# Kernel tuning notes

Hardware: AMD Instinct MI355X
Metric: run time of the kernel (lower is better)

## Reference

```python
import jax, jax.numpy as jnp
import numpy as np
from jax import lax

V, E, H, S = 50000, 512, 512, 16384


def setup_inputs() -> dict:
    key = jax.random.key(0)
    ks = jax.random.split(key, 10)
    sc_e = 1.0 / np.sqrt(E)
    sc_h = 1.0 / np.sqrt(H)
    return {
        "x": jax.random.randint(ks[0], (S,), 0, V, dtype=jnp.int64)
        if jax.config.jax_enable_x64
        else jax.random.randint(ks[0], (S,), 0, V, dtype=jnp.int32),
        "emb_table": jax.random.normal(ks[1], (V, E), dtype=jnp.float32),
        "W_ih": jax.random.uniform(ks[2], (4 * H, E), jnp.float32, -sc_h, sc_h),
        "W_hh": jax.random.uniform(ks[3], (4 * H, H), jnp.float32, -sc_h, sc_h),
        "b_ih": jax.random.uniform(ks[4], (4 * H,), jnp.float32, -sc_h, sc_h),
        "b_hh": jax.random.uniform(ks[5], (4 * H,), jnp.float32, -sc_h, sc_h),
        "W1": jax.random.uniform(ks[6], (128, H), jnp.float32, -sc_h, sc_h),
        "b1": jax.random.uniform(ks[7], (128,), jnp.float32, -sc_h, sc_h),
        "W2": jax.random.uniform(ks[8], (9, 128), jnp.float32, -1 / np.sqrt(128), 1 / np.sqrt(128)),
        "b2": jax.random.uniform(ks[9], (9,), jnp.float32, -1 / np.sqrt(128), 1 / np.sqrt(128)),
    }


def reference(x, emb_table, W_ih, W_hh, b_ih, b_hh, W1, b1, W2, b2):
    # Embedding lookup: [S, E]  (batch=1 via view(1,-1,E) in the original)
    w2v = emb_table[x]
    # Precompute input contributions to the 4 gates for all timesteps: [S, 4H]
    gx = w2v @ W_ih.T + (b_ih + b_hh)

    def step(carry, gxt):
        h, c = carry
        g = gxt + h @ W_hh.T  # [4H]; torch gate order: i, f, g, o
        i = jax.nn.sigmoid(g[:H])
        f = jax.nn.sigmoid(g[H : 2 * H])
        gg = jnp.tanh(g[2 * H : 3 * H])
        o = jax.nn.sigmoid(g[3 * H :])
        c = f * c + i * gg
        h = o * jnp.tanh(c)
        return (h, c), None

    h0 = jnp.zeros((H,), dtype=w2v.dtype)
    c0 = jnp.zeros((H,), dtype=w2v.dtype)
    (h_last, _), _ = lax.scan(step, (h0, c0), gx)

    out = jax.nn.sigmoid(h_last @ W1.T + b1)
    out = jax.nn.sigmoid(out @ W2.T + b2)
    return out[None, :]  # [1, 9], matching out[:, -1, :] batch dim
```

## Files before the change

### kernel.cpp

```cpp
#include <hip/hip_runtime.h>
#include <hip/hip_bf16.h>


#define S_LEN 16384
#define NWG   16
#define NLAUNCH 64
#define NTHR  512

typedef unsigned long long u64;
typedef float float4v __attribute__((ext_vector_type(4)));

static __device__ __forceinline__ float bf2f(unsigned int u16) {
  union { unsigned int i; float f; } v; v.i = u16 << 16; return v.f;
}
static __device__ __forceinline__ unsigned short f2bf(float f) {
  union { float f; unsigned int i; } v; v.f = f;
  unsigned int r = v.i + 0x7fffu + ((v.i >> 16) & 1u);
  return (unsigned short)(r >> 16);
}
static __device__ __forceinline__ float fsig(float x) { return 1.f / (1.f + __expf(-x)); }
static __device__ __forceinline__ float ftanh(float x) { return 2.f / (1.f + __expf(-2.f * x)) - 1.f; }

static __device__ __forceinline__ int haddr(int k) { return k + (k >> 4); }

__global__ __launch_bounds__(256, 2) void gx_gemm(
    const int* __restrict__ x, const float* __restrict__ emb,
    const float* __restrict__ W_ih, const float* __restrict__ b_ih,
    const float* __restrict__ b_hh, unsigned short* __restrict__ gx)
{
  __shared__ float As[64][40];
  __shared__ float Bs[64][40];
  __shared__ int   xs[64];

  const int tid = threadIdx.x;
  const int bm = blockIdx.x;
  const int bn = blockIdx.y;

  if (tid < 64) xs[tid] = x[bm * 64 + tid];
  __syncthreads();

  float acc[4][4] = {};
  const int r0 = (tid >> 4) * 4;
  const int c0 = tid & 15;

  for (int kc = 0; kc < 512; kc += 32) {
#pragma unroll
    for (int h = 0; h < 2; ++h) {
      const int v = tid + h * 256;
      const int row = v >> 3, k4 = v & 7;
      const float4 av = *(const float4*)(emb + (size_t)xs[row] * 512 + kc + k4 * 4);
      As[row][k4 * 4 + 0] = av.x; As[row][k4 * 4 + 1] = av.y;
      As[row][k4 * 4 + 2] = av.z; As[row][k4 * 4 + 3] = av.w;
      const float4 bv = *(const float4*)(W_ih + (size_t)(bn * 64 + row) * 512 + kc + k4 * 4);
      Bs[row][k4 * 4 + 0] = bv.x; Bs[row][k4 * 4 + 1] = bv.y;
      Bs[row][k4 * 4 + 2] = bv.z; Bs[row][k4 * 4 + 3] = bv.w;
    }
    __syncthreads();
#pragma unroll
    for (int k4 = 0; k4 < 8; ++k4) {
      float4 a[4], b[4];
#pragma unroll
      for (int i = 0; i < 4; ++i) a[i] = *(const float4*)&As[r0 + i][k4 * 4];
#pragma unroll
      for (int j = 0; j < 4; ++j) b[j] = *(const float4*)&Bs[c0 + j * 16][k4 * 4];
#pragma unroll
      for (int i = 0; i < 4; ++i)
#pragma unroll
        for (int j = 0; j < 4; ++j) {
          acc[i][j] = __builtin_fmaf(a[i].x, b[j].x, acc[i][j]);
          acc[i][j] = __builtin_fmaf(a[i].y, b[j].y, acc[i][j]);
          acc[i][j] = __builtin_fmaf(a[i].z, b[j].z, acc[i][j]);
          acc[i][j] = __builtin_fmaf(a[i].w, b[j].w, acc[i][j]);
        }
    }
    __syncthreads();
  }

#pragma unroll
  for (int j = 0; j < 4; ++j) {
    const int c = bn * 64 + c0 + j * 16;
    const float bias = b_ih[c] + b_hh[c];
    const size_t dstc = (size_t)(c & 511) * 4 + (size_t)(c >> 9);
#pragma unroll
    for (int i = 0; i < 4; ++i) {
      const size_t t = (size_t)bm * 64 + r0 + i;
      gx[t * 2048 + dstc] = f2bf(acc[i][j] + bias);
    }
  }
}

__global__ __launch_bounds__(NTHR, 1) void lstm_rec(
    const float* __restrict__ W_hh, const unsigned short* __restrict__ gx,
    const float* __restrict__ W1, const float* __restrict__ b1,
    const float* __restrict__ W2, const float* __restrict__ b2,
    float* __restrict__ out,
    unsigned int* __restrict__ h32,
    unsigned int* __restrict__ done)
{
  const int tid = threadIdx.x;
  const int w   = blockIdx.x;

  if (w >= NWG) {
    unsigned int* myflag = done + (w - NWG) * 8;
    float a0 = (float)tid, a1 = a0 + 1.f, a2 = a0 + 2.f, a3 = a0 + 3.f;
    for (;;) {
      if (__hip_atomic_load(myflag, __ATOMIC_RELAXED, __HIP_MEMORY_SCOPE_AGENT))
        break;
#pragma unroll 32
      for (int i = 0; i < 2048; ++i) {
        a0 = __builtin_fmaf(a0, 1.0000001f, 1e-9f);
        a1 = __builtin_fmaf(a1, 0.9999999f, 1e-9f);
        a2 = __builtin_fmaf(a2, 1.0000002f, 1e-9f);
        a3 = __builtin_fmaf(a3, 0.9999998f, 1e-9f);
      }
    }
    asm volatile("" :: "v"(a0), "v"(a1), "v"(a2), "v"(a3));
    return;
  }

  const int s    = tid & 31;
  const int half = (tid >> 5) & 1;
  const int wvi  = tid >> 6;
  const int ubase  = w * 32 + wvi * 4 + half * 2;
  const int ulocal = wvi * 4 + half * 2;

  float4v wvv[32];
#pragma unroll
  for (int q = 0; q < 8; ++q) {
    const int row = (q & 3) * 512 + ubase + (q >> 2);
    const float* src = W_hh + (size_t)row * 512 + s * 16;
#pragma unroll
    for (int i4 = 0; i4 < 4; ++i4) {
      asm volatile("global_load_dwordx4 %0, %1, off\n\ts_waitcnt vmcnt(0)"
                   : "=v"(wvv[q * 4 + i4]) : "v"((u64)(src + i4 * 4)) : "memory");
    }
  }

  __shared__ float hbuf[2][544];
  __shared__ unsigned int stage[32];

  float c0 = 0.f, c1 = 0.f;
  float h_reg[16];
#pragma unroll
  for (int i = 0; i < 16; ++i) h_reg[i] = 0.f;

  uint4 g_cur = {0,0,0,0}, g_nxt = {0,0,0,0};
  if (s == 0) {
    g_cur = *(const uint4*)(gx + (size_t)0 * 2048 + ubase * 4);
    g_nxt = *(const uint4*)(gx + (size_t)1 * 2048 + ubase * 4);
  }

  for (int t = 0; t < S_LEN; ++t) {
    uint4 g_new = {0,0,0,0};
    if (s == 0 && t + 2 < S_LEN)
      g_new = *(const uint4*)(gx + (size_t)(t + 2) * 2048 + ubase * 4);

    float acc[8];
#pragma unroll
    for (int q = 0; q < 8; ++q) {
      float a = 0.f;
#pragma unroll
      for (int i4 = 0; i4 < 4; ++i4) {
        const float4v vv = wvv[q * 4 + i4];
        a = __builtin_fmaf(vv.x, h_reg[i4 * 4 + 0], a);
        a = __builtin_fmaf(vv.y, h_reg[i4 * 4 + 1], a);
        a = __builtin_fmaf(vv.z, h_reg[i4 * 4 + 2], a);
        a = __builtin_fmaf(vv.w, h_reg[i4 * 4 + 3], a);
      }
      acc[q] = a;
    }
#pragma unroll
    for (int q = 0; q < 8; ++q) {
      float a = acc[q];
      a += __shfl_xor(a, 1);
      a += __shfl_xor(a, 2);
      a += __shfl_xor(a, 4);
      a += __shfl_xor(a, 8);
      a += __shfl_xor(a, 16);
      acc[q] = a;
    }

    const int buf = (t + 1) & 1;
    if (s == 0) {
      const float pi0 = acc[0] + bf2f(g_cur.x & 0xffffu);
      const float pf0 = acc[1] + bf2f(g_cur.x >> 16);
      const float pg0 = acc[2] + bf2f(g_cur.y & 0xffffu);
      const float po0 = acc[3] + bf2f(g_cur.y >> 16);
      const float pi1 = acc[4] + bf2f(g_cur.z & 0xffffu);
      const float pf1 = acc[5] + bf2f(g_cur.z >> 16);
      const float pg1 = acc[6] + bf2f(g_cur.w & 0xffffu);
      const float po1 = acc[7] + bf2f(g_cur.w >> 16);
      c0 = fsig(pf0) * c0 + fsig(pi0) * ftanh(pg0);
      c1 = fsig(pf1) * c1 + fsig(pi1) * ftanh(pg1);
      const float h0 = fsig(po0) * ftanh(c0);
      const float h1 = fsig(po1) * ftanh(c1);
      const unsigned tg16 = (unsigned)(t + 1) << 16;
      const u64 pk = ((u64)(tg16 | (unsigned)f2bf(h1)) << 32)
                   |  (u64)(tg16 | (unsigned)f2bf(h0));
      *(u64*)&stage[ulocal] = pk;
    }
    __syncthreads();

    if (tid < 64) {
      if (tid < 16) {
        const u64 sv = *(const u64*)&stage[tid * 2];
        __hip_atomic_store((u64*)&h32[buf * 512 + w * 32] + tid, sv,
                           __ATOMIC_RELAXED, __HIP_MEMORY_SCOPE_AGENT);
      }
      if (t + 1 < S_LEN) {
        const u64* hb = (const u64*)(h32 + buf * 512);
        const unsigned want = (unsigned)(t + 1) & 0xffffu;
        u64 v[4];
        for (;;) {
#pragma unroll
          for (int j = 0; j < 4; ++j)
            v[j] = __hip_atomic_load(&hb[j * 64 + tid],
                                     __ATOMIC_RELAXED, __HIP_MEMORY_SCOPE_AGENT);
          bool ok = true;
#pragma unroll
          for (int j = 0; j < 4; ++j) {
            ok &= (((unsigned)(v[j] >> 16) & 0xffffu) == want);
            ok &= ((unsigned)(v[j] >> 48) == want);
          }
          if (__all(ok)) break;
        }
#pragma unroll
        for (int j = 0; j < 4; ++j) {
          const int k = (j * 64 + tid) * 2;
          union { unsigned u; float f; } f0, f1;
          f0.u = ((unsigned)v[j]) << 16;
          f1.u = ((unsigned)(v[j] >> 32)) << 16;
          hbuf[buf][haddr(k)]     = f0.f;
          hbuf[buf][haddr(k + 1)] = f1.f;
        }
      }
    }
    __syncthreads();

    if (t + 1 < S_LEN) {
      const int base = s * 17;
#pragma unroll
      for (int i = 0; i < 16; ++i)
        h_reg[i] = hbuf[buf][base + i];
    }

    g_cur = g_nxt; g_nxt = g_new;
  }

  if (w == 0 && tid < NLAUNCH - NWG)
    __hip_atomic_store(done + tid * 8, 1u,
                       __ATOMIC_RELAXED, __HIP_MEMORY_SCOPE_AGENT);

  if (w == 0) {
    __shared__ float hl[512];
    __shared__ float zl[128];
    {
      unsigned v;
      do {
        v = __hip_atomic_load(&h32[tid], __ATOMIC_RELAXED, __HIP_MEMORY_SCOPE_AGENT);
      } while ((v >> 16) != (unsigned)S_LEN);
      union { unsigned u; float f; } hu; hu.u = v << 16;
      hl[tid] = hu.f;
    }
    __syncthreads();
    const int j = tid >> 2, q = tid & 3;
    float sum = 0.f;
    const float4* w1v = (const float4*)(W1 + (size_t)j * 512 + q * 128);
#pragma unroll 8
    for (int k4 = 0; k4 < 32; ++k4) {
      const float4 v = w1v[k4];
      const int kb = q * 128 + k4 * 4;
      sum = __builtin_fmaf(v.x, hl[kb + 0], sum);
      sum = __builtin_fmaf(v.y, hl[kb + 1], sum);
      sum = __builtin_fmaf(v.z, hl[kb + 2], sum);
      sum = __builtin_fmaf(v.w, hl[kb + 3], sum);
    }
    sum += __shfl_xor(sum, 1);
    sum += __shfl_xor(sum, 2);
    if (q == 0) zl[j] = fsig(sum + b1[j]);
    __syncthreads();
    if (tid < 9) {
      float o = b2[tid];
      const float* w2r = W2 + tid * 128;
#pragma unroll 16
      for (int k = 0; k < 128; ++k) o = __builtin_fmaf(w2r[k], zl[k], o);
      out[tid] = fsig(o);
    }
  }
}

extern "C" void kernel_launch(void* const* d_in, const int* in_sizes, int n_in,
                              void* d_out, int out_size, void* d_ws, size_t ws_size,
                              hipStream_t stream) {
  const int*   x     = (const int*)d_in[0];
  const float* emb   = (const float*)d_in[1];
  const float* W_ih  = (const float*)d_in[2];
  const float* W_hh  = (const float*)d_in[3];
  const float* b_ih  = (const float*)d_in[4];
  const float* b_hh  = (const float*)d_in[5];
  const float* W1    = (const float*)d_in[6];
  const float* b1    = (const float*)d_in[7];
  const float* W2    = (const float*)d_in[8];
  const float* b2    = (const float*)d_in[9];
  float* out = (float*)d_out;

  const size_t gx_bytes = (size_t)S_LEN * 2048 * sizeof(unsigned short);
  const size_t h_off    = gx_bytes;
  const size_t dn_off   = h_off + 4096;
  if (ws_size < h_off + 16384) return;

  unsigned short* gxp  = (unsigned short*)d_ws;
  unsigned int*   h32  = (unsigned int*)((char*)d_ws + h_off);
  unsigned int*   done = (unsigned int*)((char*)d_ws + dn_off);

  (void)hipMemsetAsync((char*)d_ws + h_off, 0, 16384, stream);

  dim3 g1(S_LEN / 64, 2048 / 64);
  gx_gemm<<<g1, 256, 0, stream>>>(x, emb, W_ih, b_ih, b_hh, gxp);
  lstm_rec<<<NLAUNCH, NTHR, 0, stream>>>(W_hh, gxp, W1, b1, W2, b2, out,
                                         h32, done);
}
```

Baseline: 44.09 ms.

## Place recurrent workgroups on stride-8 block IDs and use sc0 loads for h exchange

Result: slower. 46.33 ms (+5.1%).

```diff
diff --git a/kernel.cpp b/kernel.cpp
--- a/kernel.cpp
+++ b/kernel.cpp
@@ -4,7 +4,7 @@
 
 #define S_LEN 16384
 #define NWG   16
-#define NLAUNCH 64
+#define NLAUNCH 128
 #define NTHR  512
 
 typedef unsigned long long u64;
@@ -22,6 +22,29 @@
 static __device__ __forceinline__ float ftanh(float x) { return 2.f / (1.f + __expf(-2.f * x)) - 1.f; }
 
 static __device__ __forceinline__ int haddr(int k) { return k + (k >> 4); }
+
+static __device__ __forceinline__ u64 ld_sc0(const u64* p) {
+  u64 v;
+  asm volatile("global_load_dwordx2 %0, %1, off sc0\n\ts_waitcnt vmcnt(0)"
+               : "=v"(v) : "v"((u64)p) : "memory");
+  return v;
+}
+static __device__ __forceinline__ void st_sc0(u64* p, u64 w) {
+  asm volatile("global_store_dwordx2 %0, %1, off sc0"
+               :: "v"((u64)p), "v"(w) : "memory");
+}
+static __device__ __forceinline__ void poll4_sc0(const u64* base, int lane, u64 v[4]) {
+  u64 a = (u64)base + (u64)lane * 8ull;
+  asm volatile(
+      "global_load_dwordx2 %[v0], %[ad], off sc0\n\t"
+      "global_load_dwordx2 %[v1], %[ad], off offset:512 sc0\n\t"
+      "global_load_dwordx2 %[v2], %[ad], off offset:1024 sc0\n\t"
+      "global_load_dwordx2 %[v3], %[ad], off offset:1536 sc0\n\t"
+      "s_waitcnt vmcnt(0)"
+      : [v0] "=&v"(v[0]), [v1] "=&v"(v[1]), [v2] "=&v"(v[2]), [v3] "=&v"(v[3])
+      : [ad] "v"(a)
+      : "memory");
+}
 
 __global__ __launch_bounds__(256, 2) void gx_gemm(
     const int* __restrict__ x, const float* __restrict__ emb,
@@ -95,13 +118,16 @@
     const float* __restrict__ W2, const float* __restrict__ b2,
     float* __restrict__ out,
     unsigned int* __restrict__ h32,
+    u64* __restrict__ hs,
+    unsigned int* __restrict__ ver,
     unsigned int* __restrict__ done)
 {
   const int tid = threadIdx.x;
-  const int w   = blockIdx.x;
-
-  if (w >= NWG) {
-    unsigned int* myflag = done + (w - NWG) * 8;
+  const int wg  = blockIdx.x;
+
+  if (wg & 7) {
+    if (wg >= 64) return;
+    unsigned int* myflag = done + wg * 8;
     float a0 = (float)tid, a1 = a0 + 1.f, a2 = a0 + 2.f, a3 = a0 + 3.f;
     for (;;) {
       if (__hip_atomic_load(myflag, __ATOMIC_RELAXED, __HIP_MEMORY_SCOPE_AGENT))
@@ -118,6 +144,7 @@
     return;
   }
 
+  const int w = wg >> 3;
   const int s    = tid & 31;
   const int half = (tid >> 5) & 1;
   const int wvi  = tid >> 6;
@@ -135,6 +162,46 @@
                    : "=v"(wvv[q * 4 + i4]) : "v"((u64)(src + i4 * 4)) : "memory");
     }
   }
+
+  __shared__ int mode_sh;
+  if (tid < 64) {
+    bool fastok = true;
+    int budget = 8000;
+    for (int round = 1; round <= 4; ++round) {
+      if (tid == 0)
+        st_sc0(&hs[w], ((u64)(unsigned)round << 32) | (unsigned)w);
+      if (!fastok) continue;
+      bool ok = false;
+      while (budget > 0) {
+        --budget;
+        u64 v = 0;
+        if (tid < 16) v = ld_sc0(&hs[tid]);
+        const bool lok = (tid < 16) ? ((unsigned)(v >> 32) >= (unsigned)round) : true;
+        if (__all(lok)) { ok = true; break; }
+      }
+      if (!ok) fastok = false;
+    }
+    if (tid == 0) mode_sh = fastok ? 1 : 0;
+  }
+  __syncthreads();
+  if (tid == 0) {
+    const unsigned myfail = mode_sh ? 0u : 1u;
+    __hip_atomic_fetch_add(&ver[0], myfail, __ATOMIC_RELAXED, __HIP_MEMORY_SCOPE_AGENT);
+    __hip_atomic_fetch_add(&ver[1], 1u, __ATOMIC_RELEASE, __HIP_MEMORY_SCOPE_AGENT);
+    if (w == 0) {
+      while (__hip_atomic_load(&ver[1], __ATOMIC_ACQUIRE, __HIP_MEMORY_SCOPE_AGENT) < NWG) {}
+      const unsigned nf = __hip_atomic_load(&ver[0], __ATOMIC_RELAXED, __HIP_MEMORY_SCOPE_AGENT);
+      __hip_atomic_store(&ver[2], 0x100u | (nf == 0u ? 1u : 0u),
+                         __ATOMIC_RELAXED, __HIP_MEMORY_SCOPE_AGENT);
+    }
+    unsigned mw;
+    do {
+      mw = __hip_atomic_load(&ver[2], __ATOMIC_RELAXED, __HIP_MEMORY_SCOPE_AGENT);
+    } while (!(mw & 0x100u));
+    mode_sh = (int)(mw & 1u);
+  }
+  __syncthreads();
+  const int mode = mode_sh;
 
   __shared__ float hbuf[2][544];
   __shared__ unsigned int stage[32];
@@ -204,25 +271,39 @@
     if (tid < 64) {
       if (tid < 16) {
         const u64 sv = *(const u64*)&stage[tid * 2];
-        __hip_atomic_store((u64*)&h32[buf * 512 + w * 32] + tid, sv,
-                           __ATOMIC_RELAXED, __HIP_MEMORY_SCOPE_AGENT);
+        u64* dst = (u64*)&h32[buf * 512 + w * 32] + tid;
+        if (mode) st_sc0(dst, sv);
+        else __hip_atomic_store(dst, sv, __ATOMIC_RELAXED, __HIP_MEMORY_SCOPE_AGENT);
       }
       if (t + 1 < S_LEN) {
         const u64* hb = (const u64*)(h32 + buf * 512);
         const unsigned want = (unsigned)(t + 1) & 0xffffu;
         u64 v[4];
-        for (;;) {
-#pragma unroll
-          for (int j = 0; j < 4; ++j)
-            v[j] = __hip_atomic_load(&hb[j * 64 + tid],
-                                     __ATOMIC_RELAXED, __HIP_MEMORY_SCOPE_AGENT);
-          bool ok = true;
-#pragma unroll
-          for (int j = 0; j < 4; ++j) {
-            ok &= (((unsigned)(v[j] >> 16) & 0xffffu) == want);
-            ok &= ((unsigned)(v[j] >> 48) == want);
+        if (mode) {
+          for (;;) {
+            poll4_sc0(hb, tid, v);
+            bool ok = true;
+#pragma unroll
+            for (int j = 0; j < 4; ++j) {
+              ok &= (((unsigned)(v[j] >> 16) & 0xffffu) == want);
+              ok &= ((unsigned)(v[j] >> 48) == want);
+            }
+            if (__all(ok)) break;
           }
-          if (__all(ok)) break;
+        } else {
+          for (;;) {
+#pragma unroll
+            for (int j = 0; j < 4; ++j)
+              v[j] = __hip_atomic_load(&hb[j * 64 + tid],
+                                       __ATOMIC_RELAXED, __HIP_MEMORY_SCOPE_AGENT);
+            bool ok = true;
+#pragma unroll
+            for (int j = 0; j < 4; ++j) {
+              ok &= (((unsigned)(v[j] >> 16) & 0xffffu) == want);
+              ok &= ((unsigned)(v[j] >> 48) == want);
+            }
+            if (__all(ok)) break;
+          }
         }
 #pragma unroll
         for (int j = 0; j < 4; ++j) {
@@ -247,7 +328,7 @@
     g_cur = g_nxt; g_nxt = g_new;
   }
 
-  if (w == 0 && tid < NLAUNCH - NWG)
+  if (w == 0 && tid < 64)
     __hip_atomic_store(done + tid * 8, 1u,
                        __ATOMIC_RELAXED, __HIP_MEMORY_SCOPE_AGENT);
 
@@ -256,9 +337,18 @@
     __shared__ float zl[128];
     {
       unsigned v;
-      do {
-        v = __hip_atomic_load(&h32[tid], __ATOMIC_RELAXED, __HIP_MEMORY_SCOPE_AGENT);
-      } while ((v >> 16) != (unsigned)S_LEN);
+      if (mode) {
+        const u64* hb = (const u64*)h32;
+        u64 pv;
+        do { pv = ld_sc0(&hb[tid >> 1]); }
+        while (((unsigned)(pv >> 16) & 0xffffu) != (unsigned)S_LEN ||
+               ((unsigned)(pv >> 48)) != (unsigned)S_LEN);
+        v = (tid & 1) ? (unsigned)(pv >> 32) : (unsigned)pv;
+      } else {
+        do {
+          v = __hip_atomic_load(&h32[tid], __ATOMIC_RELAXED, __HIP_MEMORY_SCOPE_AGENT);
+        } while ((v >> 16) != (unsigned)S_LEN);
+      }
       union { unsigned u; float f; } hu; hu.u = v << 16;
       hl[tid] = hu.f;
     }
@@ -305,12 +395,16 @@
   float* out = (float*)d_out;
 
   const size_t gx_bytes = (size_t)S_LEN * 2048 * sizeof(unsigned short);
-  const size_t h_off    = gx_bytes;
-  const size_t dn_off   = h_off + 4096;
+  const size_t h_off  = gx_bytes;
+  const size_t hs_off = h_off + 4096;
+  const size_t vr_off = h_off + 4352;
+  const size_t dn_off = h_off + 4608;
   if (ws_size < h_off + 16384) return;
 
   unsigned short* gxp  = (unsigned short*)d_ws;
   unsigned int*   h32  = (unsigned int*)((char*)d_ws + h_off);
+  u64*            hsp  = (u64*)((char*)d_ws + hs_off);
+  unsigned int*   verp = (unsigned int*)((char*)d_ws + vr_off);
   unsigned int*   done = (unsigned int*)((char*)d_ws + dn_off);
 
   (void)hipMemsetAsync((char*)d_ws + h_off, 0, 16384, stream);
@@ -318,5 +412,5 @@
   dim3 g1(S_LEN / 64, 2048 / 64);
   gx_gemm<<<g1, 256, 0, stream>>>(x, emb, W_ih, b_ih, b_hh, gxp);
   lstm_rec<<<NLAUNCH, NTHR, 0, stream>>>(W_hh, gxp, W1, b1, W2, b2, out,
-                                         h32, done);
-}
+                                         h32, hsp, verp, done);
+}
```
